# Performance work log

Hardware: AMD Instinct MI355X
Metric: run time of the kernel (lower is better)

The kernel has to match this reference:

```python
import jax, jax.numpy as jnp
import numpy as np
from jax import lax

BATCH = 8192
DIM = 2048
NUM_STATES = 3


def setup_inputs() -> dict:
    key = jax.random.key(0)
    k1, k2, k3, k4 = jax.random.split(key, 4)
    y = jax.random.randint(k1, (BATCH, DIM), 0, 2, dtype=jnp.int64 if jax.config.jax_enable_x64 else jnp.int32)
    transition_probs = jax.random.normal(k2, (NUM_STATES, NUM_STATES), dtype=jnp.float32)
    emission_probs = jax.random.normal(k3, (NUM_STATES, 2), dtype=jnp.float32)
    start_probs = jax.random.normal(k4, (NUM_STATES,), dtype=jnp.float32)
    return {
        "y": y,
        "transition_probs": transition_probs,
        "emission_probs": emission_probs,
        "start_probs": start_probs,
    }


def reference(y, transition_probs, emission_probs, start_probs):
    # Normalize parameters in log space (matches torch.log_softmax)
    log_T = jax.nn.log_softmax(transition_probs, axis=-1)   # [S, S]
    log_E = jax.nn.log_softmax(emission_probs, axis=-1)     # [S, 2]
    log_pi = jax.nn.log_softmax(start_probs, axis=-1)       # [S]

    # Gather per-timestep emission log-probs: [B, DIM, S]
    em = log_E.T[y]

    # alpha_0[b, s] = log_pi[s] + log_E[s, y[b,0]]
    alpha0 = log_pi[None, :] + em[:, 0]                      # [B, S]

    def step(alpha, em_t):
        # alpha[b, i] + log_T[i, j] -> logsumexp over i, plus emission at t
        new = jax.nn.logsumexp(alpha[:, :, None] + log_T[None, :, :], axis=1) + em_t
        return new, None

    # Scan over time: em[:, 1:] moved to leading time axis -> [DIM-1, B, S]
    alpha_T, _ = lax.scan(step, alpha0, jnp.moveaxis(em[:, 1:], 1, 0))

    log_prob = jax.nn.logsumexp(alpha_T, axis=-1)            # [B]
    return log_prob.mean()
```

## Files before the change

kernel.cpp:

```cpp
#include <hip/hip_runtime.h>
#include <math.h>

#define BATCH 8192
#define DIM   2048

__global__ __launch_bounds__(256, 4)
void hmm_fwd(const int* __restrict__ y,
             const float* __restrict__ tp,
             const float* __restrict__ ep,
             const float* __restrict__ sp,
             float* __restrict__ row_lp,
             float* __restrict__ out_atomic)
{
    const int lane = threadIdx.x & 63;
    const int wid  = threadIdx.x >> 6;
    const int b    = blockIdx.x * 4 + wid;

    float T[3][3], E[3][2], pi[3];
    #pragma unroll
    for (int i = 0; i < 3; ++i) {
        float a0 = tp[i*3+0], a1 = tp[i*3+1], a2 = tp[i*3+2];
        float mx = fmaxf(a0, fmaxf(a1, a2));
        float e0 = __expf(a0-mx), e1 = __expf(a1-mx), e2 = __expf(a2-mx);
        float inv = 1.0f / (e0+e1+e2);
        T[i][0] = e0*inv; T[i][1] = e1*inv; T[i][2] = e2*inv;
    }
    #pragma unroll
    for (int s = 0; s < 3; ++s) {
        float a0 = ep[s*2+0], a1 = ep[s*2+1];
        float mx = fmaxf(a0, a1);
        float e0 = __expf(a0-mx), e1 = __expf(a1-mx);
        float inv = 1.0f / (e0+e1);
        E[s][0] = e0*inv; E[s][1] = e1*inv;
    }
    {
        float a0 = sp[0], a1 = sp[1], a2 = sp[2];
        float mx = fmaxf(a0, fmaxf(a1, a2));
        float e0 = __expf(a0-mx), e1 = __expf(a1-mx), e2 = __expf(a2-mx);
        float inv = 1.0f / (e0+e1+e2);
        pi[0] = e0*inv; pi[1] = e1*inv; pi[2] = e2*inv;
    }
    float TE0[3][3], TE1[3][3];
    #pragma unroll
    for (int k = 0; k < 3; ++k)
        #pragma unroll
        for (int j = 0; j < 3; ++j) {
            TE0[k][j] = T[k][j] * E[j][0];
            TE1[k][j] = T[k][j] * E[j][1];
        }

    const int* __restrict__ yb = y + (size_t)b * DIM;

    float R[3][3] = {{1.f,0.f,0.f},{0.f,1.f,0.f},{0.f,0.f,1.f}};
    float lsc = 0.0f;

    auto step = [&](int yv) {
        const bool one = (yv != 0);
        float nR[3][3];
        #pragma unroll
        for (int j = 0; j < 3; ++j) {
            float m0 = one ? TE1[0][j] : TE0[0][j];
            float m1 = one ? TE1[1][j] : TE0[1][j];
            float m2 = one ? TE1[2][j] : TE0[2][j];
            #pragma unroll
            for (int i = 0; i < 3; ++i)
                nR[i][j] = fmaf(R[i][0], m0, fmaf(R[i][1], m1, R[i][2]*m2));
        }
        #pragma unroll
        for (int i = 0; i < 3; ++i)
            #pragma unroll
            for (int j = 0; j < 3; ++j)
                R[i][j] = nR[i][j];
    };

    auto rescale = [&]() {
        float m = R[0][0];
        #pragma unroll
        for (int i = 0; i < 3; ++i)
            #pragma unroll
            for (int j = 0; j < 3; ++j)
                m = fmaxf(m, R[i][j]);
        lsc += __logf(m);
        float inv = 1.0f / m;
        #pragma unroll
        for (int i = 0; i < 3; ++i)
            #pragma unroll
            for (int j = 0; j < 3; ++j)
                R[i][j] *= inv;
    };

    const int tbase = lane * 32;
    #pragma unroll
    for (int g = 0; g < 8; ++g) {
        int4 q = *reinterpret_cast<const int4*>(yb + tbase + 4*g);
        if (g == 0) {
            if (lane != 0) step(q.x);
            step(q.y); step(q.z); step(q.w);
        } else {
            step(q.x); step(q.y); step(q.z); step(q.w);
        }
        if (g == 3 || g == 7) rescale();
    }

    #pragma unroll
    for (int o = 1; o < 64; o <<= 1) {
        float S[3][3];
        #pragma unroll
        for (int i = 0; i < 3; ++i)
            #pragma unroll
            for (int j = 0; j < 3; ++j)
                S[i][j] = __shfl_down(R[i][j], o, 64);
        float osc = __shfl_down(lsc, o, 64);
        float nR[3][3];
        #pragma unroll
        for (int i = 0; i < 3; ++i)
            #pragma unroll
            for (int j = 0; j < 3; ++j)
                nR[i][j] = fmaf(R[i][0], S[0][j], fmaf(R[i][1], S[1][j], R[i][2]*S[2][j]));
        #pragma unroll
        for (int i = 0; i < 3; ++i)
            #pragma unroll
            for (int j = 0; j < 3; ++j)
                R[i][j] = nR[i][j];
        lsc += osc;
    }

    if (lane == 0) {
        int y0 = yb[0];
        float a0 = pi[0] * (y0 ? E[0][1] : E[0][0]);
        float a1 = pi[1] * (y0 ? E[1][1] : E[1][0]);
        float a2 = pi[2] * (y0 ? E[2][1] : E[2][0]);
        float p = 0.0f;
        #pragma unroll
        for (int j = 0; j < 3; ++j)
            p += fmaf(a0, R[0][j], fmaf(a1, R[1][j], a2 * R[2][j]));
        float lp = __logf(p) + lsc;
        if (row_lp) row_lp[b] = lp;
        else        atomicAdd(out_atomic, lp * (1.0f / BATCH));
    }
}

__global__ void reduce_mean(const float* __restrict__ row, float* __restrict__ out)
{
    float s = 0.0f;
    for (int i = threadIdx.x; i < BATCH; i += 256) s += row[i];
    #pragma unroll
    for (int o = 32; o > 0; o >>= 1) s += __shfl_down(s, o, 64);
    __shared__ float sm[4];
    int w = threadIdx.x >> 6;
    if ((threadIdx.x & 63) == 0) sm[w] = s;
    __syncthreads();
    if (threadIdx.x == 0) out[0] = (sm[0] + sm[1] + sm[2] + sm[3]) * (1.0f / BATCH);
}

extern "C" void kernel_launch(void* const* d_in, const int* in_sizes, int n_in,
                              void* d_out, int out_size, void* d_ws, size_t ws_size,
                              hipStream_t stream)
{
    const int*   y  = (const int*)d_in[0];
    const float* tp = (const float*)d_in[1];
    const float* ep = (const float*)d_in[2];
    const float* sp = (const float*)d_in[3];
    float* out = (float*)d_out;

    const bool use_ws = (ws_size >= BATCH * sizeof(float));
    if (use_ws) {
        float* row = (float*)d_ws;
        hmm_fwd<<<BATCH/4, 256, 0, stream>>>(y, tp, ep, sp, row, nullptr);
        reduce_mean<<<1, 256, 0, stream>>>(row, out);
    } else {
        hipMemsetAsync(out, 0, sizeof(float), stream);
        hmm_fwd<<<BATCH/4, 256, 0, stream>>>(y, tp, ep, sp, nullptr, out);
    }
}
```

Before: 118.3 us.

## Precompute 4-step transition-emission matrix products in LDS lookup table

Each block builds a 24-entry shared-memory table holding products of 4 (or 3) consecutive emission-weighted transition matrices, one entry per binary observation pattern. Each lane then does one 3x3 matrix multiply per int4 of observations instead of four, with the matrix fetched from LDS by an index formed from the four bits. This cuts the serial FMA chain roughly fourfold. In exchange it adds per-block table construction, a __syncthreads, and divergent-address LDS reads. It also reuses the already loaded first observation for lane 0 instead of reloading it.

```diff
diff --git a/kernel.cpp b/kernel.cpp
--- a/kernel.cpp
+++ b/kernel.cpp
@@ -12,8 +12,11 @@
              float* __restrict__ row_lp,
              float* __restrict__ out_atomic)
 {
-    const int lane = threadIdx.x & 63;
-    const int wid  = threadIdx.x >> 6;
+    __shared__ float tbl[24 * 9];
+
+    const int tid  = threadIdx.x;
+    const int lane = tid & 63;
+    const int wid  = tid >> 6;
     const int b    = blockIdx.x * 4 + wid;
 
     float T[3][3], E[3][2], pi[3];
@@ -40,100 +43,115 @@
         float inv = 1.0f / (e0+e1+e2);
         pi[0] = e0*inv; pi[1] = e1*inv; pi[2] = e2*inv;
     }
-    float TE0[3][3], TE1[3][3];
+
+    float M0[9], M1[9];
     #pragma unroll
     for (int k = 0; k < 3; ++k)
         #pragma unroll
         for (int j = 0; j < 3; ++j) {
-            TE0[k][j] = T[k][j] * E[j][0];
-            TE1[k][j] = T[k][j] * E[j][1];
+            M0[k*3+j] = T[k][j] * E[j][0];
+            M1[k*3+j] = T[k][j] * E[j][1];
         }
 
-    const int* __restrict__ yb = y + (size_t)b * DIM;
-
-    float R[3][3] = {{1.f,0.f,0.f},{0.f,1.f,0.f},{0.f,0.f,1.f}};
-    float lsc = 0.0f;
-
-    auto step = [&](int yv) {
-        const bool one = (yv != 0);
-        float nR[3][3];
-        #pragma unroll
-        for (int j = 0; j < 3; ++j) {
-            float m0 = one ? TE1[0][j] : TE0[0][j];
-            float m1 = one ? TE1[1][j] : TE0[1][j];
-            float m2 = one ? TE1[2][j] : TE0[2][j];
+    if (tid < 24) {
+        int code, n;
+        if (tid < 16) { code = tid;      n = 4; }
+        else          { code = tid - 16; n = 3; }
+        float A[9];
+        {
+            const float* F = (code & 1) ? M1 : M0;
+            #pragma unroll
+            for (int e = 0; e < 9; ++e) A[e] = F[e];
+            code >>= 1;
+        }
+        for (int s = 1; s < n; ++s) {
+            const float* F = (code & 1) ? M1 : M0;
+            code >>= 1;
+            float Z[9];
             #pragma unroll
             for (int i = 0; i < 3; ++i)
-                nR[i][j] = fmaf(R[i][0], m0, fmaf(R[i][1], m1, R[i][2]*m2));
+                #pragma unroll
+                for (int j = 0; j < 3; ++j)
+                    Z[i*3+j] = fmaf(A[i*3+0], F[0*3+j],
+                               fmaf(A[i*3+1], F[1*3+j], A[i*3+2]*F[2*3+j]));
+            #pragma unroll
+            for (int e = 0; e < 9; ++e) A[e] = Z[e];
         }
+        #pragma unroll
+        for (int e = 0; e < 9; ++e) tbl[tid*9 + e] = A[e];
+    }
+    __syncthreads();
+
+    const int* __restrict__ yb = y + (size_t)b * DIM + lane * 32;
+
+    float R[9] = {1.f,0.f,0.f, 0.f,1.f,0.f, 0.f,0.f,1.f};
+    float lsc = 0.0f;
+    int y0 = 0;
+
+    #pragma unroll
+    for (int g = 0; g < 8; ++g) {
+        int4 q = *reinterpret_cast<const int4*>(yb + 4*g);
+        int idx;
+        if (g == 0) {
+            y0 = q.x;
+            int i4 = q.x + 2*q.y + 4*q.z + 8*q.w;
+            int i3 = 16 + (q.y + 2*q.z + 4*q.w);
+            idx = (lane == 0) ? i3 : i4;
+        } else {
+            idx = q.x + 2*q.y + 4*q.z + 8*q.w;
+        }
+        const float* __restrict__ G = &tbl[idx * 9];
+        float g0 = G[0], g1 = G[1], g2 = G[2],
+              g3 = G[3], g4 = G[4], g5 = G[5],
+              g6 = G[6], g7 = G[7], g8 = G[8];
+        float nR[9];
+        #pragma unroll
+        for (int i = 0; i < 3; ++i) {
+            nR[i*3+0] = fmaf(R[i*3+0], g0, fmaf(R[i*3+1], g3, R[i*3+2]*g6));
+            nR[i*3+1] = fmaf(R[i*3+0], g1, fmaf(R[i*3+1], g4, R[i*3+2]*g7));
+            nR[i*3+2] = fmaf(R[i*3+0], g2, fmaf(R[i*3+1], g5, R[i*3+2]*g8));
+        }
+        #pragma unroll
+        for (int e = 0; e < 9; ++e) R[e] = nR[e];
+
+        if (g == 3 || g == 7) {
+            float m = R[0];
+            #pragma unroll
+            for (int e = 1; e < 9; ++e) m = fmaxf(m, R[e]);
+            lsc += __logf(m);
+            float inv = 1.0f / m;
+            #pragma unroll
+            for (int e = 0; e < 9; ++e) R[e] *= inv;
+        }
+    }
+
+    #pragma unroll
+    for (int o = 1; o < 64; o <<= 1) {
+        float S[9];
+        #pragma unroll
+        for (int e = 0; e < 9; ++e) S[e] = __shfl_down(R[e], o, 64);
+        float osc = __shfl_down(lsc, o, 64);
+        float nR[9];
         #pragma unroll
         for (int i = 0; i < 3; ++i)
             #pragma unroll
             for (int j = 0; j < 3; ++j)
-                R[i][j] = nR[i][j];
-    };
-
-    auto rescale = [&]() {
-        float m = R[0][0];
+                nR[i*3+j] = fmaf(R[i*3+0], S[0*3+j],
+                            fmaf(R[i*3+1], S[1*3+j], R[i*3+2]*S[2*3+j]));
         #pragma unroll
-        for (int i = 0; i < 3; ++i)
-            #pragma unroll
-            for (int j = 0; j < 3; ++j)
-                m = fmaxf(m, R[i][j]);
-        lsc += __logf(m);
-        float inv = 1.0f / m;
-        #pragma unroll
-        for (int i = 0; i < 3; ++i)
-            #pragma unroll
-            for (int j = 0; j < 3; ++j)
-                R[i][j] *= inv;
-    };
-
-    const int tbase = lane * 32;
-    #pragma unroll
-    for (int g = 0; g < 8; ++g) {
-        int4 q = *reinterpret_cast<const int4*>(yb + tbase + 4*g);
-        if (g == 0) {
-            if (lane != 0) step(q.x);
-            step(q.y); step(q.z); step(q.w);
-        } else {
-            step(q.x); step(q.y); step(q.z); step(q.w);
-        }
-        if (g == 3 || g == 7) rescale();
-    }
-
-    #pragma unroll
-    for (int o = 1; o < 64; o <<= 1) {
-        float S[3][3];
-        #pragma unroll
-        for (int i = 0; i < 3; ++i)
-            #pragma unroll
-            for (int j = 0; j < 3; ++j)
-                S[i][j] = __shfl_down(R[i][j], o, 64);
-        float osc = __shfl_down(lsc, o, 64);
-        float nR[3][3];
-        #pragma unroll
-        for (int i = 0; i < 3; ++i)
-            #pragma unroll
-            for (int j = 0; j < 3; ++j)
-                nR[i][j] = fmaf(R[i][0], S[0][j], fmaf(R[i][1], S[1][j], R[i][2]*S[2][j]));
-        #pragma unroll
-        for (int i = 0; i < 3; ++i)
-            #pragma unroll
-            for (int j = 0; j < 3; ++j)
-                R[i][j] = nR[i][j];
+        for (int e = 0; e < 9; ++e) R[e] = nR[e];
         lsc += osc;
     }
 
     if (lane == 0) {
-        int y0 = yb[0];
-        float a0 = pi[0] * (y0 ? E[0][1] : E[0][0]);
-        float a1 = pi[1] * (y0 ? E[1][1] : E[1][0]);
-        float a2 = pi[2] * (y0 ? E[2][1] : E[2][0]);
+        float e0 = y0 ? E[0][1] : E[0][0];
+        float e1 = y0 ? E[1][1] : E[1][0];
+        float e2 = y0 ? E[2][1] : E[2][0];
+        float a0 = pi[0] * e0, a1 = pi[1] * e1, a2 = pi[2] * e2;
         float p = 0.0f;
         #pragma unroll
         for (int j = 0; j < 3; ++j)
-            p += fmaf(a0, R[0][j], fmaf(a1, R[1][j], a2 * R[2][j]));
+            p += fmaf(a0, R[0*3+j], fmaf(a1, R[1*3+j], a2 * R[2*3+j]));
         float lp = __logf(p) + lsc;
         if (row_lp) row_lp[b] = lp;
         else        atomicAdd(out_atomic, lp * (1.0f / BATCH));
```

Result: faster. 109.1 us (-7.8%).
